# Kernel optimization log

Measured on AMD Instinct MI355X. Metric: run time of the kernel, lower is better.

The kernel has to match this reference:

```python
import jax, jax.numpy as jnp
import numpy as np

N, E = 50000, 800000
IN_C, HID, HEADS, NUM_CLASSES = 256, 64, 4, 10
LRELU_SLOPE = 0.2
LN_EPS = 1e-5


def setup_inputs() -> dict:
    key = jax.random.key(0)
    ks = jax.random.split(key, 12)
    HC = HEADS * HID
    glorot = lambda k, shp: jax.random.normal(k, shp, jnp.float32) * np.sqrt(2.0 / (shp[0] + shp[-1]))
    return {
        "x": jax.random.normal(ks[0], (N, IN_C), jnp.float32),
        "edge_index": jax.random.randint(ks[1], (2, E), 0, N, jnp.int64),
        "edge_weight": jax.random.uniform(ks[2], (E, 1), jnp.float32),
        "W": glorot(ks[3], (IN_C, HC)),
        "att_src": glorot(ks[4], (1, HEADS, HID)),
        "att_dst": glorot(ks[5], (1, HEADS, HID)),
        "att_edge": glorot(ks[6], (1, HEADS, HID)),
        "W_edge": glorot(ks[7], (1, HC)),
        "bias": jnp.zeros((HC,), jnp.float32),
        "ln_gamma": jnp.ones((HC,), jnp.float32),
        "ln_beta": jnp.zeros((HC,), jnp.float32),
        "fc_W": glorot(ks[8], (HC, NUM_CLASSES)),
        "fc_b": jnp.zeros((NUM_CLASSES,), jnp.float32),
    }


def reference(x, edge_index, edge_weight, W, att_src, att_dst, att_edge,
              W_edge, bias, ln_gamma, ln_beta, fc_W, fc_b):
    n = x.shape[0]
    src, dst = edge_index[0], edge_index[1]

    # GATConv: linear projection -> [N, H, C]
    xh = (x @ W).reshape(n, HEADS, HID)
    a_src = jnp.sum(xh * att_src, axis=-1)  # [N, H]
    a_dst = jnp.sum(xh * att_dst, axis=-1)  # [N, H]

    # edge feature projection (edge_dim=1) -> per-edge attention term
    eh = (edge_weight @ W_edge).reshape(-1, HEADS, HID)  # [E, H, C]
    a_edge = jnp.sum(eh * att_edge, axis=-1)             # [E, H]

    alpha = a_src[src] + a_dst[dst] + a_edge             # [E, H]
    alpha = jax.nn.leaky_relu(alpha, LRELU_SLOPE)

    # segment softmax over incoming edges of each destination node
    amax = jax.ops.segment_max(alpha, dst, num_segments=n)  # [N, H]
    amax = jnp.where(jnp.isfinite(amax), amax, 0.0)
    ex = jnp.exp(alpha - amax[dst])
    esum = jax.ops.segment_sum(ex, dst, num_segments=n)     # [N, H]
    attn = ex / (esum[dst] + 1e-16)                          # [E, H]

    # message = gathered source features weighted by attention; scatter-add
    msg = xh[src] * attn[:, :, None]                          # [E, H, C]
    out = jax.ops.segment_sum(msg, dst, num_segments=n)      # [N, H, C]
    out = out.reshape(n, HEADS * HID) + bias                  # concat heads

    # LayerNorm + ReLU (dropout is identity in eval) + Linear head
    mu = jnp.mean(out, axis=-1, keepdims=True)
    var = jnp.mean(jnp.square(out - mu), axis=-1, keepdims=True)
    out = (out - mu) * jax.lax.rsqrt(var + LN_EPS) * ln_gamma + ln_beta
    out = jax.nn.relu(out)
    return out @ fc_W + fc_b
```

## Files before the change

### kernel.cpp

```cpp
#include <hip/hip_runtime.h>
#include <hip/hip_bf16.h>

static constexpr int HEADS = 4;
static constexpr int HID   = 64;
static constexpr int HC    = 256;
static constexpr int NCLS  = 10;

typedef short    bf16x8 __attribute__((ext_vector_type(8)));
typedef _Float16 f16x8  __attribute__((ext_vector_type(8)));
typedef _Float16 f16x4  __attribute__((ext_vector_type(4)));
typedef float    f32x4  __attribute__((ext_vector_type(4)));

__device__ inline unsigned short f2bf(float f) {
    union { float f; unsigned u; } c; c.f = f;
    unsigned r = (c.u + 0x7fff + ((c.u >> 16) & 1)) >> 16;
    return (unsigned short)r;
}
__device__ inline unsigned short f2h(float f) {
    _Float16 h = (_Float16)f; unsigned short u; __builtin_memcpy(&u, &h, 2); return u;
}
__device__ inline float h2f(unsigned short u) {
    _Float16 h; __builtin_memcpy(&h, &u, 2); return (float)h;
}

__global__ void prep_kernel(const float* __restrict__ We, const float* __restrict__ attE,
                            float* __restrict__ cE, const float* __restrict__ W,
                            unsigned short* __restrict__ Wt, const float* __restrict__ fcW,
                            unsigned short* __restrict__ fcWh, int* __restrict__ deg,
                            int Nn) {
    int b = blockIdx.x, t = threadIdx.x;
    if (b == 0) {
        float p = We[t] * attE[t];
#pragma unroll
        for (int d = 32; d; d >>= 1) p += __shfl_xor(p, d, 64);
        if ((t & 63) == 0) cE[t >> 6] = p;
    } else if (b <= 256) {
        int k = b - 1;
        Wt[t * 256 + k] = f2bf(W[k * 256 + t]);
    } else if (b <= 272) {
        int j = b - 257;
        unsigned short v = 0;
        if (j < NCLS) v = f2h(fcW[t * NCLS + j]);
        fcWh[j * 256 + t] = v;
    } else {
        int i = (b - 273) * 256 + t;
        if (i < Nn) deg[i] = 0;
    }
}

__global__ __launch_bounds__(256) void gemm_mfma(const float* __restrict__ X,
                                                 const unsigned short* __restrict__ Bt,
                                                 unsigned short* __restrict__ XHh, int M) {
    __shared__ alignas(16) unsigned short As[128][40];
    __shared__ alignas(16) unsigned short Bs[128][40];
    const int tid = threadIdx.x;
    const int lane = tid & 63, wid = tid >> 6;
    const int wr = wid >> 1, wc = wid & 1;
    const int bm = blockIdx.x * 128, bn = blockIdx.y * 128;
    const int fr = lane & 15, kg = lane >> 4;

    f32x4 acc[4][4] = {};

    for (int k0 = 0; k0 < 256; k0 += 32) {
        __syncthreads();
#pragma unroll
        for (int ss = 0; ss < 4; ++ss) {
            int idx = tid + (ss << 8);
            int row = idx >> 3, seg = idx & 7;
            int grow = bm + row;
            float4 av = make_float4(0.f, 0.f, 0.f, 0.f);
            if (grow < M) av = *(const float4*)&X[(size_t)grow * 256 + k0 + seg * 4];
            ushort4 ab = make_ushort4(f2bf(av.x), f2bf(av.y), f2bf(av.z), f2bf(av.w));
            *(ushort4*)&As[row][seg * 4] = ab;
        }
#pragma unroll
        for (int qq = 0; qq < 2; ++qq) {
            int q = tid + (qq << 8);
            int row = q >> 2, part = q & 3;
            const ushort4* bp = (const ushort4*)&Bt[(size_t)(bn + row) * 256 + k0 + part * 8];
            *(ushort4*)&Bs[row][part * 8]     = bp[0];
            *(ushort4*)&Bs[row][part * 8 + 4] = bp[1];
        }
        __syncthreads();

        bf16x8 af[4], bf[4];
#pragma unroll
        for (int i = 0; i < 4; ++i)
            af[i] = *(const bf16x8*)&As[wr * 64 + i * 16 + fr][kg * 8];
#pragma unroll
        for (int j = 0; j < 4; ++j)
            bf[j] = *(const bf16x8*)&Bs[wc * 64 + j * 16 + fr][kg * 8];
#pragma unroll
        for (int i = 0; i < 4; ++i)
#pragma unroll
            for (int j = 0; j < 4; ++j)
                acc[i][j] = __builtin_amdgcn_mfma_f32_16x16x32_bf16(af[i], bf[j], acc[i][j], 0, 0, 0);
    }

#pragma unroll
    for (int i = 0; i < 4; ++i) {
#pragma unroll
        for (int j = 0; j < 4; ++j) {
            int col = bn + wc * 64 + j * 16 + fr;
#pragma unroll
            for (int r = 0; r < 4; ++r) {
                int row = bm + wr * 64 + i * 16 + kg * 4 + r;
                if (row < M) XHh[(size_t)row * 256 + col] = f2h(acc[i][j][r]);
            }
        }
    }
}

__global__ __launch_bounds__(256) void attn_coef(const unsigned short* __restrict__ xhh,
                                                 const float* __restrict__ attS,
                                                 const float* __restrict__ attD,
                                                 float* __restrict__ a_src,
                                                 float* __restrict__ a_dst,
                                                 int Nn) {
    int wid = threadIdx.x >> 6, lane = threadIdx.x & 63;
    int n = blockIdx.x * 4 + wid;
    if (n >= Nn) return;
    ushort4 xv = *(const ushort4*)&xhh[(size_t)n * HC + lane * 4];
    float x0 = h2f(xv.x), x1 = h2f(xv.y), x2 = h2f(xv.z), x3 = h2f(xv.w);
    float4 sv = *(const float4*)&attS[lane * 4];
    float4 dv = *(const float4*)&attD[lane * 4];
    float ps = x0 * sv.x + x1 * sv.y + x2 * sv.z + x3 * sv.w;
    float pd = x0 * dv.x + x1 * dv.y + x2 * dv.z + x3 * dv.w;
#pragma unroll
    for (int d = 1; d < 16; d <<= 1) {
        ps += __shfl_xor(ps, d, 64);
        pd += __shfl_xor(pd, d, 64);
    }
    if ((lane & 15) == 0) {
        a_src[n * 4 + (lane >> 4)] = ps;
        a_dst[n * 4 + (lane >> 4)] = pd;
    }
}

__global__ void hist_kernel(const int* __restrict__ dst, int* __restrict__ deg,
                            int* __restrict__ rank, int E) {
    int e = blockIdx.x * 256 + threadIdx.x;
    if (e < E) rank[e] = atomicAdd(&deg[dst[e]], 1);
}

__global__ __launch_bounds__(1024) void scan1(const int* __restrict__ deg,
                                              int* __restrict__ row_start,
                                              int* __restrict__ bsum, int n) {
    __shared__ int wsum[16];
    const int tid = threadIdx.x, lane = tid & 63, wid = tid >> 6;
    int i = blockIdx.x * 1024 + tid;
    int v = (i < n) ? ((deg[i] + 3) & ~3) : 0;
    int incl = v;
#pragma unroll
    for (int d = 1; d < 64; d <<= 1) {
        int t = __shfl_up(incl, d, 64);
        if (lane >= d) incl += t;
    }
    if (lane == 63) wsum[wid] = incl;
    __syncthreads();
    if (tid < 16) {
        int w = wsum[tid];
#pragma unroll
        for (int d = 1; d < 16; d <<= 1) {
            int t = __shfl_up(w, d, 16);
            if (tid >= d) w += t;
        }
        wsum[tid] = w;
    }
    __syncthreads();
    int waveoff = wid ? wsum[wid - 1] : 0;
    if (i < n) row_start[i] = waveoff + incl - v;
    if (tid == 1023) bsum[blockIdx.x] = waveoff + incl;
}

__global__ __launch_bounds__(1024) void scan23(int* __restrict__ row_start,
                                               const int* __restrict__ bsum,
                                               const int* __restrict__ deg,
                                               int2* __restrict__ sew, int n, int nb) {
    __shared__ int pref[64];
    const int tid = threadIdx.x;
    if (tid < 64) {
        int v = (tid < nb) ? bsum[tid] : 0;
#pragma unroll
        for (int d = 1; d < 64; d <<= 1) {
            int t = __shfl_up(v, d, 64);
            if (tid >= d) v += t;
        }
        pref[tid] = v;
    }
    __syncthreads();
    int add = blockIdx.x ? pref[blockIdx.x - 1] : 0;
    int i = blockIdx.x * 1024 + tid;
    if (i < n) {
        int v = row_start[i] + add;
        row_start[i] = v;
        int dn = deg[i];
        int pd = (dn + 3) & ~3;
        for (int s = dn; s < pd; ++s) sew[v + s] = make_int2(0, 0);
    }
    if (i == n) row_start[n] = pref[nb - 1];
}

__global__ void scatter_sw(const int* __restrict__ src, const int* __restrict__ dst,
                           const float* __restrict__ ew,
                           const int* __restrict__ row_start, const int* __restrict__ rank,
                           int2* __restrict__ sew, int E) {
    int e = blockIdx.x * 256 + threadIdx.x;
    if (e >= E) return;
    int pos = row_start[dst[e]] + rank[e];
    sew[pos] = make_int2(src[e], __float_as_int(ew[e]));
}

__global__ __launch_bounds__(256) void p_pass(
    const int* __restrict__ row_start, const int* __restrict__ deg,
    const int2* __restrict__ sew, const float* __restrict__ a_src,
    const float* __restrict__ a_dst, const float* __restrict__ cE,
    int* __restrict__ srcs, float* __restrict__ pq, int Nn) {
    const int wid = threadIdx.x >> 6, lane = threadIdx.x & 63;
    const int n = blockIdx.x * 4 + wid;
    if (n >= Nn) return;
    const int rs = row_start[n];
    const int dn = deg[n];
    const int pd = (dn + 3) & ~3;
    const int slot0 = lane >> 2, h = lane & 3;
    const float adn = a_dst[n * 4 + h];
    const float ceh = cE[h];
    for (int s = slot0; s < pd; s += 16) {
        int pos = rs + s;
        int2 r = sew[pos];
        float p = 0.f;
        if (s < dn) {
            float a = a_src[r.x * 4 + h] + adn + ceh * __int_as_float(r.y);
            a = fmaxf(a, 0.2f * a);
            p = __expf(a);
        }
        if (h == 0) srcs[pos] = r.x;
        pq[(size_t)(pos >> 2) * 16 + h * 4 + (pos & 3)] = p;
    }
}

__global__ __launch_bounds__(256) void gat_main(
    const unsigned short* __restrict__ xhh, const int* __restrict__ row_start,
    const int* __restrict__ srcs, const float* __restrict__ pq,
    const float* __restrict__ bias, const float* __restrict__ gamma,
    const float* __restrict__ beta, unsigned short* __restrict__ yh, int Nn) {
    __shared__ alignas(16) f32x4 s_acc[2][64];
    __shared__ float s_ps[2][64];

    const int lane = threadIdx.x & 63, wid = threadIdx.x >> 6;
    const int nslot = wid >> 1, sub = wid & 1;
    const int n = blockIdx.x * 2 + nslot;
    const int myh = lane >> 4;
    const unsigned short* xl = xhh + (size_t)lane * 4;

    f32x4 acc = {0.f, 0.f, 0.f, 0.f};
    float psum = 0.f;

    if (n < Nn) {
        const int rs = row_start[n], re = row_start[n + 1];
        const int rs4 = rs >> 2;
        const int G = (re - rs) >> 2;
        const int myG = (G - sub + 1) >> 1;

#define LOADMETA(c, S, P)                                                     \
    S = *(const int4*)&srcs[(rs4 + (c)) * 4];                                 \
    P = *(const float4*)&pq[((size_t)(rs4 + (c))) * 16 + myh * 4];
#define GATHER(S, X0, X1, X2, X3)                                             \
    X0 = *(const f16x4*)(xl + (size_t)__builtin_amdgcn_readfirstlane((S).x) * HC); \
    X1 = *(const f16x4*)(xl + (size_t)__builtin_amdgcn_readfirstlane((S).y) * HC); \
    X2 = *(const f16x4*)(xl + (size_t)__builtin_amdgcn_readfirstlane((S).z) * HC); \
    X3 = *(const f16x4*)(xl + (size_t)__builtin_amdgcn_readfirstlane((S).w) * HC);
#define COMPUTE(P, X0, X1, X2, X3)                                            \
    psum += ((P).x + (P).y) + ((P).z + (P).w);                                \
    acc[0] = fmaf((P).x, (float)(X0).x, acc[0]);                              \
    acc[1] = fmaf((P).x, (float)(X0).y, acc[1]);                              \
    acc[2] = fmaf((P).x, (float)(X0).z, acc[2]);                              \
    acc[3] = fmaf((P).x, (float)(X0).w, acc[3]);                              \
    acc[0] = fmaf((P).y, (float)(X1).x, acc[0]);                              \
    acc[1] = fmaf((P).y, (float)(X1).y, acc[1]);                              \
    acc[2] = fmaf((P).y, (float)(X1).z, acc[2]);                              \
    acc[3] = fmaf((P).y, (float)(X1).w, acc[3]);                              \
    acc[0] = fmaf((P).z, (float)(X2).x, acc[0]);                              \
    acc[1] = fmaf((P).z, (float)(X2).y, acc[1]);                              \
    acc[2] = fmaf((P).z, (float)(X2).z, acc[2]);                              \
    acc[3] = fmaf((P).z, (float)(X2).w, acc[3]);                              \
    acc[0] = fmaf((P).w, (float)(X3).x, acc[0]);                              \
    acc[1] = fmaf((P).w, (float)(X3).y, acc[1]);                              \
    acc[2] = fmaf((P).w, (float)(X3).z, acc[2]);                              \
    acc[3] = fmaf((P).w, (float)(X3).w, acc[3]);

        if (myG > 0) {
            int4 s0, sN = {0, 0, 0, 0}, s2 = {0, 0, 0, 0};
            float4 pC, pN = {0.f, 0.f, 0.f, 0.f}, p2 = {0.f, 0.f, 0.f, 0.f};
            f16x4 g0, g1, g2, g3;
            LOADMETA(sub, s0, pC);
            GATHER(s0, g0, g1, g2, g3);
            if (myG > 1) { LOADMETA(sub + 2, sN, pN); }
            for (int k = 0; k < myG; ++k) {
                f16x4 h0, h1, h2, h3;
                if (k + 1 < myG) { GATHER(sN, h0, h1, h2, h3); }
                if (k + 2 < myG) { LOADMETA(sub + 2 * (k + 2), s2, p2); }
                COMPUTE(pC, g0, g1, g2, g3);
                pC = pN; pN = p2; sN = s2;
                g0 = h0; g1 = h1; g2 = h2; g3 = h3;
            }
        }
#undef LOADMETA
#undef GATHER
#undef COMPUTE
    }

    if (sub == 1) { s_acc[nslot][lane] = acc; s_ps[nslot][lane] = psum; }
    __syncthreads();
    if (sub == 1 || n >= Nn) return;
    f32x4 oacc = s_acc[nslot][lane];
    acc[0] += oacc[0]; acc[1] += oacc[1]; acc[2] += oacc[2]; acc[3] += oacc[3];
    psum += s_ps[nslot][lane];

    float rin = 1.f / (psum + 1e-16f);

    float4 bv = *(const float4*)&bias[lane * 4];
    float v0 = acc[0] * rin + bv.x;
    float v1 = acc[1] * rin + bv.y;
    float v2 = acc[2] * rin + bv.z;
    float v3 = acc[3] * rin + bv.w;

    float s1 = v0 + v1 + v2 + v3;
    float s2v = v0 * v0 + v1 * v1 + v2 * v2 + v3 * v3;
#pragma unroll
    for (int d = 1; d < 64; d <<= 1) {
        s1 += __shfl_xor(s1, d, 64);
        s2v += __shfl_xor(s2v, d, 64);
    }
    float mu = s1 * (1.f / 256.f);
    float var = s2v * (1.f / 256.f) - mu * mu;
    float rstd = rsqrtf(var + 1e-5f);
    float4 gv = *(const float4*)&gamma[lane * 4];
    float4 btv = *(const float4*)&beta[lane * 4];
    float y0 = fmaxf((v0 - mu) * rstd * gv.x + btv.x, 0.f);
    float y1 = fmaxf((v1 - mu) * rstd * gv.y + btv.y, 0.f);
    float y2 = fmaxf((v2 - mu) * rstd * gv.z + btv.z, 0.f);
    float y3 = fmaxf((v3 - mu) * rstd * gv.w + btv.w, 0.f);

    f16x4 yv;
    yv.x = (_Float16)y0; yv.y = (_Float16)y1; yv.z = (_Float16)y2; yv.w = (_Float16)y3;
    *(f16x4*)&yh[(size_t)n * HC + lane * 4] = yv;
}

__global__ __launch_bounds__(256) void fc_gemm(const unsigned short* __restrict__ yh,
                                               const unsigned short* __restrict__ fcWh,
                                               const float* __restrict__ fcb,
                                               float* __restrict__ out, int M) {
    const int lane = threadIdx.x & 63, wid = threadIdx.x >> 6;
    const int rowbase = blockIdx.x * 256 + wid * 64;
    const int fr = lane & 15, kg = lane >> 4;
    f32x4 acc[4] = {};
#pragma unroll
    for (int k0 = 0; k0 < 256; k0 += 32) {
        f16x8 bfr = *(const f16x8*)&fcWh[fr * 256 + k0 + kg * 8];
#pragma unroll
        for (int i = 0; i < 4; ++i) {
            int row = rowbase + i * 16 + fr;
            f16x8 afr = {};
            if (row < M) afr = *(const f16x8*)&yh[(size_t)row * 256 + k0 + kg * 8];
            acc[i] = __builtin_amdgcn_mfma_f32_16x16x32_f16(afr, bfr, acc[i], 0, 0, 0);
        }
    }
    if (fr < NCLS) {
        float bb = fcb[fr];
#pragma unroll
        for (int i = 0; i < 4; ++i) {
#pragma unroll
            for (int r = 0; r < 4; ++r) {
                int row = rowbase + i * 16 + kg * 4 + r;
                if (row < M) out[(size_t)row * NCLS + fr] = acc[i][r] + bb;
            }
        }
    }
}

extern "C" void kernel_launch(void* const* d_in, const int* in_sizes, int n_in,
                              void* d_out, int out_size, void* d_ws, size_t ws_size,
                              hipStream_t stream) {
    const float* x    = (const float*)d_in[0];
    const int*   ei   = (const int*)d_in[1];
    const float* ew   = (const float*)d_in[2];
    const float* W    = (const float*)d_in[3];
    const float* attS = (const float*)d_in[4];
    const float* attD = (const float*)d_in[5];
    const float* attE = (const float*)d_in[6];
    const float* We   = (const float*)d_in[7];
    const float* bias = (const float*)d_in[8];
    const float* gam  = (const float*)d_in[9];
    const float* bet  = (const float*)d_in[10];
    const float* fcW  = (const float*)d_in[11];
    const float* fcb  = (const float*)d_in[12];
    float* out = (float*)d_out;

    const int Nn = in_sizes[0] / HC;
    const int E  = in_sizes[1] / 2;
    const int* src = ei;
    const int* dst = ei + E;
    const int nb = (Nn + 1023) / 1024;
    const int EpMax = E + 4 * Nn;

    char* ws = (char*)d_ws;
    size_t off = 0;
    auto alloc = [&](size_t bytes) { void* p = ws + off; off = (off + bytes + 255) & ~size_t(255); return p; };
    unsigned short* xhh  = (unsigned short*)alloc((size_t)Nn * HC * 2);
    unsigned short* yh   = (unsigned short*)alloc((size_t)Nn * HC * 2);
    unsigned short* wt   = (unsigned short*)alloc((size_t)HC * HC * 2);
    unsigned short* fcWh = (unsigned short*)alloc((size_t)16 * HC * 2);
    float* a_srcb    = (float*)alloc((size_t)Nn * 4 * 4);
    float* a_dstb    = (float*)alloc((size_t)Nn * 4 * 4);
    float* cE        = (float*)alloc(256);
    int*   row_start = (int*)  alloc((size_t)(Nn + 1) * 4);
    int*   deg       = (int*)  alloc((size_t)Nn * 4);
    int*   bsum      = (int*)  alloc((size_t)nb * 4);
    int*   rank      = (int*)  alloc((size_t)E * 4);
    int2*  sew       = (int2*) alloc((size_t)EpMax * 8 + 256);
    int*   srcs      = (int*)  alloc((size_t)EpMax * 4 + 256);
    float* pq        = (float*)alloc((size_t)EpMax * 16 + 1024);
    (void)ws_size;

    prep_kernel<<<273 + (Nn + 255) / 256, 256, 0, stream>>>(We, attE, cE, W, wt,
                                                            fcW, fcWh, deg, Nn);

    dim3 g((Nn + 127) / 128, 2);
    gemm_mfma<<<g, 256, 0, stream>>>(x, wt, xhh, Nn);

    attn_coef<<<(Nn + 3) / 4, 256, 0, stream>>>(xhh, attS, attD, a_srcb, a_dstb, Nn);
    hist_kernel<<<(E + 255) / 256, 256, 0, stream>>>(dst, deg, rank, E);
    scan1<<<nb, 1024, 0, stream>>>(deg, row_start, bsum, Nn);
    scan23<<<nb, 1024, 0, stream>>>(row_start, bsum, deg, sew, Nn, nb);
    scatter_sw<<<(E + 255) / 256, 256, 0, stream>>>(src, dst, ew, row_start, rank,
                                                    sew, E);
    p_pass<<<(Nn + 3) / 4, 256, 0, stream>>>(row_start, deg, sew,
                                             a_srcb, a_dstb, cE, srcs, pq, Nn);
    gat_main<<<(Nn + 1) / 2, 256, 0, stream>>>(xhh, row_start, srcs, pq,
                                               bias, gam, bet, yh, Nn);
    fc_gemm<<<(Nn + 255) / 256, 256, 0, stream>>>(yh, fcWh, fcb, out, Nn);
}
```

Baseline: 198.8 us.

## Normalize attention in p_pass and accumulate gat_main in packed fp16

p_pass now makes two passes over each node's edges. The first computes the softmax denominator and the second stores fp16 attention weights, packed and duplicated into 32-bit words. gat_main switches from two waves per node with an LDS reduction to one wave per node. It uses a deeper 4-stage metadata/gather software pipeline and packed fp16 FMA accumulation, and scan23 no longer zero-fills padding slots. This removes the cross-wave sync and the fp32 conversion work, at the cost of fp16 accumulation precision and recomputing the exp terms in p_pass.

```diff
diff --git a/kernel.cpp b/kernel.cpp
--- a/kernel.cpp
+++ b/kernel.cpp
@@ -9,6 +9,7 @@
 typedef short    bf16x8 __attribute__((ext_vector_type(8)));
 typedef _Float16 f16x8  __attribute__((ext_vector_type(8)));
 typedef _Float16 f16x4  __attribute__((ext_vector_type(4)));
+typedef _Float16 f16x2  __attribute__((ext_vector_type(2)));
 typedef float    f32x4  __attribute__((ext_vector_type(4)));
 
 __device__ inline unsigned short f2bf(float f) {
@@ -21,6 +22,17 @@
 }
 __device__ inline float h2f(unsigned short u) {
     _Float16 h; __builtin_memcpy(&h, &u, 2); return (float)h;
+}
+__device__ inline f16x2 u2h2(unsigned u) {
+    union { unsigned u; f16x2 h; } c; c.u = u; return c.h;
+}
+
+__device__ inline void edge_acc(unsigned aw, f16x4 X, f16x2& a0, f16x2& a1) {
+    f16x2 a  = u2h2(aw);
+    f16x2 lo = __builtin_shufflevector(X, X, 0, 1);
+    f16x2 hi = __builtin_shufflevector(X, X, 2, 3);
+    a0 = a * lo + a0;
+    a1 = a * hi + a1;
 }
 
 __global__ void prep_kernel(const float* __restrict__ We, const float* __restrict__ attE,
@@ -174,9 +186,7 @@
 }
 
 __global__ __launch_bounds__(1024) void scan23(int* __restrict__ row_start,
-                                               const int* __restrict__ bsum,
-                                               const int* __restrict__ deg,
-                                               int2* __restrict__ sew, int n, int nb) {
+                                               const int* __restrict__ bsum, int n, int nb) {
     __shared__ int pref[64];
     const int tid = threadIdx.x;
     if (tid < 64) {
@@ -191,13 +201,7 @@
     __syncthreads();
     int add = blockIdx.x ? pref[blockIdx.x - 1] : 0;
     int i = blockIdx.x * 1024 + tid;
-    if (i < n) {
-        int v = row_start[i] + add;
-        row_start[i] = v;
-        int dn = deg[i];
-        int pd = (dn + 3) & ~3;
-        for (int s = dn; s < pd; ++s) sew[v + s] = make_int2(0, 0);
-    }
+    if (i < n) row_start[i] += add;
     if (i == n) row_start[n] = pref[nb - 1];
 }
 
@@ -215,7 +219,7 @@
     const int* __restrict__ row_start, const int* __restrict__ deg,
     const int2* __restrict__ sew, const float* __restrict__ a_src,
     const float* __restrict__ a_dst, const float* __restrict__ cE,
-    int* __restrict__ srcs, float* __restrict__ pq, int Nn) {
+    int* __restrict__ srcs, unsigned* __restrict__ pq, int Nn) {
     const int wid = threadIdx.x >> 6, lane = threadIdx.x & 63;
     const int n = blockIdx.x * 4 + wid;
     if (n >= Nn) return;
@@ -225,105 +229,125 @@
     const int slot0 = lane >> 2, h = lane & 3;
     const float adn = a_dst[n * 4 + h];
     const float ceh = cE[h];
+
+    float esum = 0.f;
+    for (int s = slot0; s < dn; s += 16) {
+        int2 r = sew[rs + s];
+        float a = a_src[r.x * 4 + h] + adn + ceh * __int_as_float(r.y);
+        a = fmaxf(a, 0.2f * a);
+        esum += __expf(a);
+    }
+#pragma unroll
+    for (int d = 4; d < 64; d <<= 1) esum += __shfl_xor(esum, d, 64);
+    float rin = 1.f / (esum + 1e-16f);
+
     for (int s = slot0; s < pd; s += 16) {
         int pos = rs + s;
-        int2 r = sew[pos];
-        float p = 0.f;
+        float at = 0.f;
+        int sv = 0;
         if (s < dn) {
+            int2 r = sew[pos];
+            sv = r.x;
             float a = a_src[r.x * 4 + h] + adn + ceh * __int_as_float(r.y);
             a = fmaxf(a, 0.2f * a);
-            p = __expf(a);
-        }
-        if (h == 0) srcs[pos] = r.x;
-        pq[(size_t)(pos >> 2) * 16 + h * 4 + (pos & 3)] = p;
+            at = __expf(a) * rin;
+        }
+        if (h == 0) srcs[pos] = sv;
+        unsigned ah = f2h(at);
+        pq[(size_t)(pos >> 2) * 16 + h * 4 + (pos & 3)] = ah | (ah << 16);
     }
 }
 
 __global__ __launch_bounds__(256) void gat_main(
     const unsigned short* __restrict__ xhh, const int* __restrict__ row_start,
-    const int* __restrict__ srcs, const float* __restrict__ pq,
+    const int* __restrict__ srcs, const unsigned* __restrict__ pqw,
     const float* __restrict__ bias, const float* __restrict__ gamma,
     const float* __restrict__ beta, unsigned short* __restrict__ yh, int Nn) {
-    __shared__ alignas(16) f32x4 s_acc[2][64];
-    __shared__ float s_ps[2][64];
-
     const int lane = threadIdx.x & 63, wid = threadIdx.x >> 6;
-    const int nslot = wid >> 1, sub = wid & 1;
-    const int n = blockIdx.x * 2 + nslot;
+    const int n = blockIdx.x * 4 + wid;
+    if (n >= Nn) return;
     const int myh = lane >> 4;
-    const unsigned short* xl = xhh + (size_t)lane * 4;
-
-    f32x4 acc = {0.f, 0.f, 0.f, 0.f};
-    float psum = 0.f;
-
-    if (n < Nn) {
-        const int rs = row_start[n], re = row_start[n + 1];
-        const int rs4 = rs >> 2;
-        const int G = (re - rs) >> 2;
-        const int myG = (G - sub + 1) >> 1;
-
-#define LOADMETA(c, S, P)                                                     \
-    S = *(const int4*)&srcs[(rs4 + (c)) * 4];                                 \
-    P = *(const float4*)&pq[((size_t)(rs4 + (c))) * 16 + myh * 4];
-#define GATHER(S, X0, X1, X2, X3)                                             \
-    X0 = *(const f16x4*)(xl + (size_t)__builtin_amdgcn_readfirstlane((S).x) * HC); \
-    X1 = *(const f16x4*)(xl + (size_t)__builtin_amdgcn_readfirstlane((S).y) * HC); \
-    X2 = *(const f16x4*)(xl + (size_t)__builtin_amdgcn_readfirstlane((S).z) * HC); \
-    X3 = *(const f16x4*)(xl + (size_t)__builtin_amdgcn_readfirstlane((S).w) * HC);
-#define COMPUTE(P, X0, X1, X2, X3)                                            \
-    psum += ((P).x + (P).y) + ((P).z + (P).w);                                \
-    acc[0] = fmaf((P).x, (float)(X0).x, acc[0]);                              \
-    acc[1] = fmaf((P).x, (float)(X0).y, acc[1]);                              \
-    acc[2] = fmaf((P).x, (float)(X0).z, acc[2]);                              \
-    acc[3] = fmaf((P).x, (float)(X0).w, acc[3]);                              \
-    acc[0] = fmaf((P).y, (float)(X1).x, acc[0]);                              \
-    acc[1] = fmaf((P).y, (float)(X1).y, acc[1]);                              \
-    acc[2] = fmaf((P).y, (float)(X1).z, acc[2]);                              \
-    acc[3] = fmaf((P).y, (float)(X1).w, acc[3]);                              \
-    acc[0] = fmaf((P).z, (float)(X2).x, acc[0]);                              \
-    acc[1] = fmaf((P).z, (float)(X2).y, acc[1]);                              \
-    acc[2] = fmaf((P).z, (float)(X2).z, acc[2]);                              \
-    acc[3] = fmaf((P).z, (float)(X2).w, acc[3]);                              \
-    acc[0] = fmaf((P).w, (float)(X3).x, acc[0]);                              \
-    acc[1] = fmaf((P).w, (float)(X3).y, acc[1]);                              \
-    acc[2] = fmaf((P).w, (float)(X3).z, acc[2]);                              \
-    acc[3] = fmaf((P).w, (float)(X3).w, acc[3]);
-
-        if (myG > 0) {
-            int4 s0, sN = {0, 0, 0, 0}, s2 = {0, 0, 0, 0};
-            float4 pC, pN = {0.f, 0.f, 0.f, 0.f}, p2 = {0.f, 0.f, 0.f, 0.f};
-            f16x4 g0, g1, g2, g3;
-            LOADMETA(sub, s0, pC);
-            GATHER(s0, g0, g1, g2, g3);
-            if (myG > 1) { LOADMETA(sub + 2, sN, pN); }
-            for (int k = 0; k < myG; ++k) {
-                f16x4 h0, h1, h2, h3;
-                if (k + 1 < myG) { GATHER(sN, h0, h1, h2, h3); }
-                if (k + 2 < myG) { LOADMETA(sub + 2 * (k + 2), s2, p2); }
-                COMPUTE(pC, g0, g1, g2, g3);
-                pC = pN; pN = p2; sN = s2;
-                g0 = h0; g1 = h1; g2 = h2; g3 = h3;
+    const int rs = row_start[n], re = row_start[n + 1];
+    const int rs4 = rs >> 2;
+    const int G = (re - rs) >> 2;
+
+    f16x2 acc0 = {(_Float16)0, (_Float16)0};
+    f16x2 acc1 = {(_Float16)0, (_Float16)0};
+
+    int4  ms0 = {}, ms1 = {}, ms2 = {}, ms3 = {};
+    uint4 mp0 = {}, mp1 = {}, mp2 = {}, mp3 = {};
+    f16x4 A0 = {}, A1 = {}, A2 = {}, A3 = {};
+    f16x4 B0 = {}, B1 = {}, B2 = {}, B3 = {};
+
+#define META(i, c_) do {                                                       \
+    ms##i = *(const int4*)(srcs + ((size_t)(rs4 + (c_)) << 2));                \
+    mp##i = *(const uint4*)(pqw + ((size_t)(rs4 + (c_)) << 4) + (myh << 2));   \
+} while (0)
+#define ROW(D, sv_) do {                                                       \
+    unsigned sb_ = __builtin_amdgcn_readfirstlane((unsigned)(sv_));            \
+    const f16x4* rp_ = (const f16x4*)(xhh + (size_t)sb_ * HC);                 \
+    D = rp_[lane];                                                             \
+} while (0)
+#define GATH(S, i) do {                                                        \
+    ROW(S##0, ms##i.x); ROW(S##1, ms##i.y);                                    \
+    ROW(S##2, ms##i.z); ROW(S##3, ms##i.w);                                    \
+} while (0)
+#define COMP(S, i) do {                                                        \
+    edge_acc(mp##i.x, S##0, acc0, acc1);                                       \
+    edge_acc(mp##i.y, S##1, acc0, acc1);                                       \
+    edge_acc(mp##i.z, S##2, acc0, acc1);                                       \
+    edge_acc(mp##i.w, S##3, acc0, acc1);                                       \
+} while (0)
+
+    if (G > 0) {
+        META(0, 0); GATH(A, 0);
+        if (G > 1) { META(1, 1); GATH(B, 1); }
+        if (G > 2) META(2, 2);
+        if (G > 3) META(3, 3);
+        int c = 0;
+        for (; c + 8 <= G; c += 4) {
+            COMP(A, 0); GATH(A, 2); META(0, c + 4);
+            COMP(B, 1); GATH(B, 3); META(1, c + 5);
+            COMP(A, 2); GATH(A, 0); META(2, c + 6);
+            COMP(B, 3); GATH(B, 1); META(3, c + 7);
+        }
+        int R = G - c;
+        COMP(A, 0);
+        if (c + 2 < G) GATH(A, 2);
+        if (c + 4 < G) META(0, c + 4);
+        if (R > 1) {
+            COMP(B, 1);
+            if (c + 3 < G) GATH(B, 3);
+            if (c + 5 < G) META(1, c + 5);
+            if (R > 2) {
+                COMP(A, 2);
+                if (c + 4 < G) GATH(A, 0);
+                if (c + 6 < G) META(2, c + 6);
+                if (R > 3) {
+                    COMP(B, 3);
+                    if (c + 5 < G) GATH(B, 1);
+                    if (R > 4) {
+                        COMP(A, 0);
+                        if (c + 6 < G) GATH(A, 2);
+                        if (R > 5) {
+                            COMP(B, 1);
+                            if (R > 6) COMP(A, 2);
+                        }
+                    }
+                }
             }
         }
-#undef LOADMETA
-#undef GATHER
-#undef COMPUTE
-    }
-
-    if (sub == 1) { s_acc[nslot][lane] = acc; s_ps[nslot][lane] = psum; }
-    __syncthreads();
-    if (sub == 1 || n >= Nn) return;
-    f32x4 oacc = s_acc[nslot][lane];
-    acc[0] += oacc[0]; acc[1] += oacc[1]; acc[2] += oacc[2]; acc[3] += oacc[3];
-    psum += s_ps[nslot][lane];
-
-    float rin = 1.f / (psum + 1e-16f);
+    }
+#undef META
+#undef ROW
+#undef GATH
+#undef COMP
 
     float4 bv = *(const float4*)&bias[lane * 4];
-    float v0 = acc[0] * rin + bv.x;
-    float v1 = acc[1] * rin + bv.y;
-    float v2 = acc[2] * rin + bv.z;
-    float v3 = acc[3] * rin + bv.w;
+    float v0 = (float)acc0[0] + bv.x;
+    float v1 = (float)acc0[1] + bv.y;
+    float v2 = (float)acc1[0] + bv.z;
+    float v3 = (float)acc1[1] + bv.w;
 
     float s1 = v0 + v1 + v2 + v3;
     float s2v = v0 * v0 + v1 * v1 + v2 * v2 + v3 * v3;
@@ -343,7 +367,8 @@
     float y3 = fmaxf((v3 - mu) * rstd * gv.w + btv.w, 0.f);
 
     f16x4 yv;
-    yv.x = (_Float16)y0; yv.y = (_Float16)y1; yv.z = (_Float16)y2; yv.w = (_Float16)y3;
+    yv[0] = (_Float16)y0; yv[1] = (_Float16)y1;
+    yv[2] = (_Float16)y2; yv[3] = (_Float16)y3;
     *(f16x4*)&yh[(size_t)n * HC + lane * 4] = yv;
 }
 
@@ -420,7 +445,7 @@
     int*   rank      = (int*)  alloc((size_t)E * 4);
     int2*  sew       = (int2*) alloc((size_t)EpMax * 8 + 256);
     int*   srcs      = (int*)  alloc((size_t)EpMax * 4 + 256);
-    float* pq        = (float*)alloc((size_t)EpMax * 16 + 1024);
+    unsigned* pq     = (unsigned*)alloc((size_t)EpMax * 16 + 1024);
     (void)ws_size;
 
     prep_kernel<<<273 + (Nn + 255) / 256, 256, 0, stream>>>(We, attE, cE, W, wt,
@@ -432,12 +457,12 @@
     attn_coef<<<(Nn + 3) / 4, 256, 0, stream>>>(xhh, attS, attD, a_srcb, a_dstb, Nn);
     hist_kernel<<<(E + 255) / 256, 256, 0, stream>>>(dst, deg, rank, E);
     scan1<<<nb, 1024, 0, stream>>>(deg, row_start, bsum, Nn);
-    scan23<<<nb, 1024, 0, stream>>>(row_start, bsum, deg, sew, Nn, nb);
+    scan23<<<nb, 1024, 0, stream>>>(row_start, bsum, Nn, nb);
     scatter_sw<<<(E + 255) / 256, 256, 0, stream>>>(src, dst, ew, row_start, rank,
                                                     sew, E);
     p_pass<<<(Nn + 3) / 4, 256, 0, stream>>>(row_start, deg, sew,
                                              a_srcb, a_dstb, cE, srcs, pq, Nn);
-    gat_main<<<(Nn + 1) / 2, 256, 0, stream>>>(xhh, row_start, srcs, pq,
+    gat_main<<<(Nn + 3) / 4, 256, 0, stream>>>(xhh, row_start, srcs, pq,
                                                bias, gam, bet, yh, Nn);
     fc_gemm<<<(Nn + 255) / 256, 256, 0, stream>>>(yh, fcWh, fcb, out, Nn);
 }
```

Result: no change. 199.8 us (+0.5%).
